# Optimization experiments

Hardware: AMD Instinct MI355X
Metric: run time of the kernel (lower is better)

Reference implementation:

```python
import jax, jax.numpy as jnp
import numpy as np
from jax import lax

POOL_OUT = 20  # SOCA AdaptiveAvgPool2d((20,20))
MID = 16       # out_channel // 2
BN_EPS = 1e-3


def _pool_matrix(n, out):
    # Row-stochastic matrix replicating torch AdaptiveAvgPool2d bin boundaries:
    # start = floor(i*n/out), end = ceil((i+1)*n/out)
    P = np.zeros((out, n), np.float32)
    for i in range(out):
        s = (i * n) // out
        e = -((-(i + 1) * n) // out)
        P[i, s:e] = 1.0 / (e - s)
    return jnp.asarray(P)


def setup_inputs() -> dict:
    key = jax.random.key(0)
    ks = jax.random.split(key, 5)
    B, C, H, W = 16, 256, 128, 128
    OC = 32
    x = jax.random.normal(ks[0], (B, C, H, W), dtype=jnp.float32)
    linear_w = jax.random.normal(ks[1], (C, C), dtype=jnp.float32) * (1.0 / np.sqrt(C))
    linear_b = jnp.zeros((C,), jnp.float32)
    lsa_w = jax.random.normal(ks[2], (1, 2, 7, 7), dtype=jnp.float32) * 0.1  # Conv2d(2,1,7) no bias
    conv_w = jax.random.normal(ks[3], (OC, OC, 3, 3), dtype=jnp.float32) * (1.0 / np.sqrt(OC * 9))
    conv_b = jnp.zeros((OC,), jnp.float32)
    bn_gamma = jnp.ones((OC,), jnp.float32)
    bn_beta = jnp.zeros((OC,), jnp.float32)
    return {"x": x, "linear_w": linear_w, "linear_b": linear_b, "lsa_w": lsa_w,
            "conv_w": conv_w, "conv_b": conv_b, "bn_gamma": bn_gamma, "bn_beta": bn_beta}


def _bsa_forward(x, linear_w, linear_b, lsa_w, conv_w, conv_b, bn_gamma, bn_beta):
    b, c, h, w = x.shape
    # ---- SOCA: second-order channel attention ----
    PH = _pool_matrix(h, POOL_OUT)
    PW = _pool_matrix(w, POOL_OUT)
    xp = jnp.einsum('oh,bchw,pw->bcop', PH, x, PW)          # (b,c,20,20)
    n = POOL_OUT * POOL_OUT
    v = xp.reshape(b, c, n).transpose(0, 2, 1)               # (b,400,c)
    vc = v - v.mean(axis=1, keepdims=True)
    cov = jnp.einsum('bnc,bnd->bcd', vc, vc) / (n - 1)       # (b,c,c)
    feat = cov.mean(axis=2)                                  # (b,c)
    attn = jax.nn.sigmoid(feat @ linear_w.T + linear_b)      # (b,c)
    # ---- channel scoring / top-k selection ----
    score = attn.mean(axis=0)                                # (c,)
    score_id = jnp.argsort(-score)                           # descending
    max_id = jnp.sort(score_id[:MID])                        # (MID,)
    x1 = jnp.take(x, max_id, axis=1) * (1.0 + score[max_id])[None, :, None, None]
    # ---- grouped channel mean (c divisible by MID by construction) ----
    g = c // MID
    x2 = x.reshape(b, MID, g, h, w).mean(axis=2)             # (b,MID,h,w)
    xc = jnp.concatenate([x1, x2], axis=1)                   # (b,32,h,w)
    # ---- LSA spatial attention ----
    s = jnp.concatenate([xc.mean(axis=1, keepdims=True),
                         xc.max(axis=1, keepdims=True)], axis=1)  # (b,2,h,w)
    a = lax.conv_general_dilated(s, lsa_w, (1, 1), [(3, 3), (3, 3)],
                                 dimension_numbers=('NCHW', 'OIHW', 'NCHW'))
    xa = xc * jax.nn.sigmoid(a)
    # ---- CBA: conv(3x3, stride 2) + BN(train stats) + SiLU ----
    y = lax.conv_general_dilated(xa, conv_w, (2, 2), [(1, 1), (1, 1)],
                                 dimension_numbers=('NCHW', 'OIHW', 'NCHW'))
    y = y + conv_b[None, :, None, None]
    mu = y.mean(axis=(0, 2, 3))
    var = y.var(axis=(0, 2, 3))
    yn = (y - mu[None, :, None, None]) * lax.rsqrt(var + BN_EPS)[None, :, None, None]
    yn = yn * bn_gamma[None, :, None, None] + bn_beta[None, :, None, None]
    return yn * jax.nn.sigmoid(yn)  # SiLU


def reference(x, linear_w, linear_b, lsa_w, conv_w, conv_b, bn_gamma, bn_beta):
    return _bsa_forward(x, linear_w, linear_b, lsa_w, conv_w, conv_b, bn_gamma, bn_beta)
```

## Files before the change

### kernel.cpp

```cpp
#include <hip/hip_runtime.h>
#include <math.h>

#define B_ 16
#define C_ 256
#define H_ 128
#define W_ 128
#define HW_ (H_*W_)
#define PO 20
#define NPOOL (PO*PO)
#define MID_ 16
#define OC_ 32
#define OH_ 64
#define OW_ 64
#define BN_EPS 1e-3f

#define OFF_XP     0
#define OFF_SN     1638400
#define OFF_FEAT   1644800
#define OFF_SCORE  1648896
#define OFF_MAXID  1649152
#define OFF_SCALE  1649168
#define OFF_BNSUM  1649184
#define OFF_BNSQ   1649216
#define OFF_SMEAN  1649248
#define OFF_SMAX   1911392
#define OFF_SIGA   2173536
#define OFF_XC     2435680

__device__ __forceinline__ int bin_s(int p) { return (p * 128) / 20; }
__device__ __forceinline__ int bin_e(int p) { return ((p + 1) * 128 + 19) / 20; }

__global__ __launch_bounds__(256) void k_pool2(const float* __restrict__ x,
                                               float* __restrict__ xp,
                                               float* __restrict__ sn,
                                               float* __restrict__ xc) {
  __shared__ float tmp[2][64 * 21];
  const int blk = blockIdx.x;
  const int b = blk >> 5, g = (blk >> 1) & 15, rh = blk & 1;
  const int tid = threadIdx.x;
  const int hl = tid >> 2, q = tid & 3;
  const int hg = rh * 64 + hl;
  const float* rowbase = x + (size_t)(b * C_) * HW_ + (size_t)hg * W_ + q * 32;

  float4 xacc[8];
#pragma unroll
  for (int j = 0; j < 8; ++j) xacc[j] = make_float4(0.f, 0.f, 0.f, 0.f);
  float snacc = 0.f;

  for (int k = 0; k < 16; ++k) {
    const int c = g * 16 + k;
    const float4* src4 = (const float4*)(rowbase + (size_t)c * HW_);
    float bin[5];
#pragma unroll
    for (int p = 0; p < 5; ++p) bin[p] = 0.f;
#pragma unroll
    for (int j = 0; j < 8; ++j) {
      float4 v = src4[j];
      xacc[j].x += v.x; xacc[j].y += v.y; xacc[j].z += v.z; xacc[j].w += v.w;
      const float c4[4] = {v.x, v.y, v.z, v.w};
#pragma unroll
      for (int kk = 0; kk < 4; ++kk) {
        const int cc = 4 * j + kk;
#pragma unroll
        for (int p = 0; p < 5; ++p) {
          const int S = (p * 32) / 5;
          const int E = ((p + 1) * 32 + 4) / 5;
          if (cc >= S && cc < E) bin[p] += c4[kk];
        }
      }
    }
    float* tb = tmp[k & 1];
#pragma unroll
    for (int p = 0; p < 5; ++p) {
      const int S = (p * 32) / 5, E = ((p + 1) * 32 + 4) / 5;
      tb[hl * 21 + q * 5 + p] = bin[p] / (float)(E - S);
    }
    __syncthreads();
    if (tid < 200) {
      const int ol = tid / 20, p = tid % 20;
      const int o = rh * 10 + ol;
      const int rs = bin_s(o), re = bin_e(o);
      float s = 0.f;
      for (int r = rs; r < re; ++r) s += tb[(r - rh * 64) * 21 + p];
      float v = s / (float)(re - rs);
      xp[(size_t)(b * C_ + c) * NPOOL + o * PO + p] = v;
      snacc += v;
    }
  }
  if (tid < 200) atomicAdd(&sn[b * NPOOL + rh * 200 + tid], snacc);
  float4* dst = (float4*)(xc + (size_t)(b * OC_ + MID_ + g) * HW_ + (size_t)hg * W_ + q * 32);
#pragma unroll
  for (int j = 0; j < 8; ++j) {
    float4 v = xacc[j];
    v.x *= 0.0625f; v.y *= 0.0625f; v.z *= 0.0625f; v.w *= 0.0625f;
    dst[j] = v;
  }
}

__global__ __launch_bounds__(256) void k_feat(const float* __restrict__ xp,
                                              const float* __restrict__ sn,
                                              float* __restrict__ feat) {
  const int b = blockIdx.x;
  const int tid = threadIdx.x;
  __shared__ float snl[NPOOL];
  __shared__ float red[256];
  const float4* row4 = (const float4*)(xp + (size_t)(b * C_ + tid) * NPOOL);
  for (int i = tid; i < NPOOL; i += 256) snl[i] = sn[b * NPOOL + i];
  float rs = 0.f;
#pragma unroll 4
  for (int n = 0; n < NPOOL / 4; ++n) {
    float4 v = row4[n];
    rs += v.x + v.y + v.z + v.w;
  }
  red[tid] = rs;
  __syncthreads();
  for (int s = 128; s > 0; s >>= 1) {
    if (tid < s) red[tid] += red[tid + s];
    __syncthreads();
  }
  const float totm = red[0] / (float)NPOOL;
  __syncthreads();
  float sl = 0.f;
  for (int i = tid; i < NPOOL; i += 256) sl += snl[i];
  red[tid] = sl;
  __syncthreads();
  for (int s = 128; s > 0; s >>= 1) {
    if (tid < s) red[tid] += red[tid + s];
    __syncthreads();
  }
  const float S = red[0] - (float)NPOOL * totm;
  float dot = 0.f;
#pragma unroll 4
  for (int n4 = 0; n4 < NPOOL / 4; ++n4) {
    float4 v = row4[n4];
    dot += v.x * snl[4 * n4] + v.y * snl[4 * n4 + 1]
         + v.z * snl[4 * n4 + 2] + v.w * snl[4 * n4 + 3];
  }
  const float m = rs / (float)NPOOL;
  feat[b * C_ + tid] = (dot - totm * rs - m * S) / ((float)(NPOOL - 1) * (float)C_);
}

__global__ __launch_bounds__(256) void k_attn(const float* __restrict__ feat,
                                              const float* __restrict__ lw,
                                              const float* __restrict__ lb,
                                              float* __restrict__ score) {
  __shared__ float sf[B_ * 257];
  __shared__ float wc[16 * 257];
  __shared__ float zs[16 * 17];
  const int tid = threadIdx.x;
  const int j0 = blockIdx.x * 16;
  for (int i = tid; i < B_ * C_; i += 256) sf[(i >> 8) * 257 + (i & 255)] = feat[i];
  for (int i = tid; i < 16 * C_; i += 256)
    wc[(i >> 8) * 257 + (i & 255)] = lw[(size_t)(j0 + (i >> 8)) * C_ + (i & 255)];
  __syncthreads();
  const int jl = tid >> 4, bb = tid & 15;
  float z = 0.f;
#pragma unroll 8
  for (int i = 0; i < C_; ++i) z += sf[bb * 257 + i] * wc[jl * 257 + i];
  z += lb[j0 + jl];
  zs[jl * 17 + bb] = 1.0f / (1.0f + expf(-z));
  __syncthreads();
  if (tid < 16) {
    float s = 0.f;
#pragma unroll
    for (int k = 0; k < 16; ++k) s += zs[tid * 17 + k];
    score[j0 + tid] = s / (float)B_;
  }
}

__global__ __launch_bounds__(256) void k_select(const float* __restrict__ score,
                                                int* __restrict__ max_id,
                                                float* __restrict__ scale,
                                                float* __restrict__ bnzero) {
  __shared__ float ss[C_];
  __shared__ int flag[C_];
  const int tid = threadIdx.x;
  if (tid < 64) bnzero[tid] = 0.f;
  ss[tid] = score[tid];
  __syncthreads();
  float my = ss[tid];
  int rank = 0;
  for (int k = 0; k < C_; ++k) {
    float v = ss[k];
    rank += (v > my || (v == my && k < tid)) ? 1 : 0;
  }
  flag[tid] = (rank < MID_) ? 1 : 0;
  __syncthreads();
  if (rank < MID_) {
    int pos = 0;
    for (int k = 0; k < tid; ++k) pos += flag[k];
    max_id[pos] = tid;
    scale[pos] = 1.0f + my;
  }
}

__global__ __launch_bounds__(256) void k_build(const float* __restrict__ x,
                                               const int* __restrict__ max_id,
                                               const float* __restrict__ scale,
                                               float* __restrict__ xc,
                                               float* __restrict__ smean,
                                               float* __restrict__ smax) {
  __shared__ int mid_s[MID_];
  __shared__ float sc_s[MID_];
  __shared__ float4 ps[128], pm[128];
  const int tid = threadIdx.x;
  if (tid < MID_) {
    mid_s[tid] = max_id[tid];
    sc_s[tid] = scale[tid];
  }
  __syncthreads();
  const int p = tid & 127, s = tid >> 7;
  const int P = blockIdx.x * 128 + p;
  const int b = P >> 12, pix4 = P & 4095;
  const float4* xb = (const float4*)x + (size_t)(b * C_) * (HW_ / 4) + pix4;
  float4* xcb = (float4*)xc + (size_t)(b * OC_) * (HW_ / 4) + pix4;
  float4 ms = make_float4(0.f, 0.f, 0.f, 0.f);
  float4 mx = make_float4(-INFINITY, -INFINITY, -INFINITY, -INFINITY);
#pragma unroll
  for (int mi = 0; mi < 8; ++mi) {
    int m = s * 8 + mi;
    float4 t = xb[(size_t)mid_s[m] * (HW_ / 4)];
    float sc = sc_s[m];
    t.x *= sc; t.y *= sc; t.z *= sc; t.w *= sc;
    xcb[(size_t)m * (HW_ / 4)] = t;
    ms.x += t.x; ms.y += t.y; ms.z += t.z; ms.w += t.w;
    mx.x = fmaxf(mx.x, t.x); mx.y = fmaxf(mx.y, t.y);
    mx.z = fmaxf(mx.z, t.z); mx.w = fmaxf(mx.w, t.w);
  }
#pragma unroll
  for (int gi = 0; gi < 8; ++gi) {
    float4 t = xcb[(size_t)(MID_ + s * 8 + gi) * (HW_ / 4)];
    ms.x += t.x; ms.y += t.y; ms.z += t.z; ms.w += t.w;
    mx.x = fmaxf(mx.x, t.x); mx.y = fmaxf(mx.y, t.y);
    mx.z = fmaxf(mx.z, t.z); mx.w = fmaxf(mx.w, t.w);
  }
  if (s == 1) { ps[p] = ms; pm[p] = mx; }
  __syncthreads();
  if (s == 0) {
    float4 a = ps[p], m2 = pm[p];
    ms.x = (ms.x + a.x) * (1.f / 32.f); ms.y = (ms.y + a.y) * (1.f / 32.f);
    ms.z = (ms.z + a.z) * (1.f / 32.f); ms.w = (ms.w + a.w) * (1.f / 32.f);
    mx.x = fmaxf(mx.x, m2.x); mx.y = fmaxf(mx.y, m2.y);
    mx.z = fmaxf(mx.z, m2.z); mx.w = fmaxf(mx.w, m2.w);
    ((float4*)smean)[P] = ms;
    ((float4*)smax)[P] = mx;
  }
}

__global__ __launch_bounds__(256) void k_lsa(const float* __restrict__ smean,
                                             const float* __restrict__ smax,
                                             const float* __restrict__ lsa_w,
                                             float* __restrict__ siga) {
  __shared__ float w0[49], w1[49];
  if (threadIdx.x < 49) {
    w0[threadIdx.x] = lsa_w[threadIdx.x];
    w1[threadIdx.x] = lsa_w[49 + threadIdx.x];
  }
  __syncthreads();
  int idx = blockIdx.x * 256 + threadIdx.x;
  int b = idx >> 14;
  int pix = idx & (HW_ - 1);
  int h = pix >> 7, w = pix & 127;
  const float* pm = smean + (size_t)b * HW_;
  const float* px = smax + (size_t)b * HW_;
  float acc = 0.f;
  for (int kh = 0; kh < 7; ++kh) {
    int ih = h + kh - 3;
    if (ih < 0 || ih >= H_) continue;
    for (int kw = 0; kw < 7; ++kw) {
      int iw = w + kw - 3;
      if (iw < 0 || iw >= W_) continue;
      int p = ih * W_ + iw;
      acc += pm[p] * w0[kh * 7 + kw] + px[p] * w1[kh * 7 + kw];
    }
  }
  siga[idx] = 1.0f / (1.0f + __expf(-acc));
}

__global__ __launch_bounds__(256) void k_conv(const float* __restrict__ xc,
                                              const float* __restrict__ siga,
                                              const float* __restrict__ conv_w,
                                              const float* __restrict__ conv_b,
                                              float* __restrict__ out,
                                              float* __restrict__ bnsum,
                                              float* __restrict__ bnsq) {
  __shared__ __attribute__((aligned(16))) float in_lds[4 * 5 * 132];
  __shared__ float sg_lds[5 * 132];
  __shared__ float w_lds[288 * 32];
  const int tid = threadIdx.x;
  const int oc = tid & 31;
  const int g = tid >> 5;
  const int b = blockIdx.x >> 5;
  const int oh0 = (blockIdx.x & 31) * 2;
  const int ih0 = 2 * oh0 - 1;

  for (int i = tid; i < 288 * 32; i += 256) {
    int oc_ = i / 288, rem = i % 288;
    w_lds[rem * 32 + oc_] = conv_w[i];
  }
  const float* sgb = siga + (size_t)b * HW_;
  for (int i = tid; i < 5 * 132; i += 256) {
    int r = i / 132, col = i % 132;
    int ih = ih0 + r, iw = col - 1;
    float v = 0.f;
    if (ih >= 0 && ih < H_ && iw >= 0 && iw < W_) v = sgb[ih * W_ + iw];
    sg_lds[i] = v;
  }

  float acc[2][8];
#pragma unroll
  for (int a = 0; a < 2; ++a)
#pragma unroll
    for (int o = 0; o < 8; ++o) acc[a][o] = 0.f;

  for (int chunk = 0; chunk < 8; ++chunk) {
    __syncthreads();
    for (int i = tid; i < 4 * 5 * 132; i += 256) {
      int icl = i / 660;
      int rem = i % 660;
      int r = rem / 132, col = rem % 132;
      int ih = ih0 + r, iw = col - 1;
      float v = 0.f;
      if (ih >= 0 && ih < H_ && iw >= 0 && iw < W_) {
        v = xc[((size_t)(b * OC_) + (chunk * 4 + icl)) * HW_ + ih * W_ + iw] * sg_lds[rem];
      }
      in_lds[i] = v;
    }
    __syncthreads();
#pragma unroll
    for (int icl = 0; icl < 4; ++icl) {
      const int wb = (chunk * 4 + icl) * 9 * 32 + oc;
#pragma unroll
      for (int r = 0; r < 5; ++r) {
        float f[20] __attribute__((aligned(16)));
        const float4* s4 = (const float4*)&in_lds[(icl * 5 + r) * 132 + 16 * g];
#pragma unroll
        for (int j = 0; j < 5; ++j) ((float4*)f)[j] = s4[j];
#pragma unroll
        for (int ohl = 0; ohl < 2; ++ohl) {
          const int kh = r - 2 * ohl;
          if (kh < 0 || kh > 2) continue;
          float w0 = w_lds[wb + (kh * 3 + 0) * 32];
          float w1 = w_lds[wb + (kh * 3 + 1) * 32];
          float w2 = w_lds[wb + (kh * 3 + 2) * 32];
#pragma unroll
          for (int o = 0; o < 8; ++o)
            acc[ohl][o] += f[2 * o] * w0 + f[2 * o + 1] * w1 + f[2 * o + 2] * w2;
        }
      }
    }
  }

  float bias = conv_b[oc];
  float lsum = 0.f, lsq = 0.f;
  float* outp = out + ((size_t)(b * OC_) + oc) * (OH_ * OW_) + (size_t)oh0 * OW_ + g * 8;
#pragma unroll
  for (int ohl = 0; ohl < 2; ++ohl) {
    float vout[8] __attribute__((aligned(16)));
#pragma unroll
    for (int o = 0; o < 8; ++o) {
      float v = acc[ohl][o] + bias;
      vout[o] = v;
      lsum += v;
      lsq += v * v;
    }
    *((float4*)(outp + ohl * OW_)) = *(float4*)&vout[0];
    *((float4*)(outp + ohl * OW_ + 4)) = *(float4*)&vout[4];
  }
  __syncthreads();
  in_lds[tid] = lsum;
  in_lds[256 + tid] = lsq;
  __syncthreads();
  if (tid < 32) {
    float t = 0.f, tq = 0.f;
#pragma unroll
    for (int gg = 0; gg < 8; ++gg) {
      t += in_lds[gg * 32 + tid];
      tq += in_lds[256 + gg * 32 + tid];
    }
    atomicAdd(&bnsum[tid], t);
    atomicAdd(&bnsq[tid], tq);
  }
}

__global__ __launch_bounds__(256) void k_apply(float* __restrict__ out,
                                               const float* __restrict__ sum,
                                               const float* __restrict__ sq,
                                               const float* __restrict__ gamma,
                                               const float* __restrict__ beta) {
  __shared__ float ssc[OC_], ssh[OC_];
  if (threadIdx.x < OC_) {
    int i = threadIdx.x;
    const float N = (float)(B_ * OH_ * OW_);
    float mu = sum[i] / N;
    float var = sq[i] / N - mu * mu;
    float sc = gamma[i] / sqrtf(var + BN_EPS);
    ssc[i] = sc;
    ssh[i] = beta[i] - mu * sc;
  }
  __syncthreads();
  int idx4 = blockIdx.x * 256 + threadIdx.x;
  int oc = (idx4 >> 10) & 31;
  float sc = ssc[oc], sh = ssh[oc];
  float4 v = ((float4*)out)[idx4];
  float t;
  t = v.x * sc + sh; v.x = t / (1.0f + __expf(-t));
  t = v.y * sc + sh; v.y = t / (1.0f + __expf(-t));
  t = v.z * sc + sh; v.z = t / (1.0f + __expf(-t));
  t = v.w * sc + sh; v.w = t / (1.0f + __expf(-t));
  ((float4*)out)[idx4] = v;
}

extern "C" void kernel_launch(void* const* d_in, const int* in_sizes, int n_in,
                              void* d_out, int out_size, void* d_ws, size_t ws_size,
                              hipStream_t stream) {
  const float* x      = (const float*)d_in[0];
  const float* lw     = (const float*)d_in[1];
  const float* lb     = (const float*)d_in[2];
  const float* lsa_w  = (const float*)d_in[3];
  const float* conv_w = (const float*)d_in[4];
  const float* conv_b = (const float*)d_in[5];
  const float* gamma  = (const float*)d_in[6];
  const float* beta   = (const float*)d_in[7];
  float* out = (float*)d_out;
  float* ws = (float*)d_ws;

  hipMemsetAsync(ws + OFF_SN, 0, B_ * NPOOL * sizeof(float), stream);

  k_pool2<<<512, 256, 0, stream>>>(x, ws + OFF_XP, ws + OFF_SN, ws + OFF_XC);
  k_feat<<<B_, 256, 0, stream>>>(ws + OFF_XP, ws + OFF_SN, ws + OFF_FEAT);
  k_attn<<<16, 256, 0, stream>>>(ws + OFF_FEAT, lw, lb, ws + OFF_SCORE);
  k_select<<<1, 256, 0, stream>>>(ws + OFF_SCORE, (int*)(ws + OFF_MAXID),
                                  ws + OFF_SCALE, ws + OFF_BNSUM);
  k_build<<<512, 256, 0, stream>>>(x, (const int*)(ws + OFF_MAXID), ws + OFF_SCALE,
                                   ws + OFF_XC, ws + OFF_SMEAN, ws + OFF_SMAX);
  k_lsa<<<1024, 256, 0, stream>>>(ws + OFF_SMEAN, ws + OFF_SMAX, lsa_w, ws + OFF_SIGA);
  k_conv<<<512, 256, 0, stream>>>(ws + OFF_XC, ws + OFF_SIGA, conv_w, conv_b, out,
                                  ws + OFF_BNSUM, ws + OFF_BNSQ);
  k_apply<<<2048, 256, 0, stream>>>(out, ws + OFF_BNSUM, ws + OFF_BNSQ, gamma, beta);
}
```

Before: 517.7 us.

## Fuse feat/attn/select kernels, prefetch pooling loads, pad conv weight LDS

Merges the covariance-feature and linear/sigmoid attention kernels into one per-batch kernel that accumulates the score with atomics. It also moves top-k selection into every k_build block, which removes two tiny launches but repeats the rank computation in 512 blocks. The pooling kernel now software-prefetches the next channel's rows into registers and uses a lighter barrier. The conv kernel pads its weight LDS to stride 33 and caches the 9 taps in registers. A single memset now zeroes the sn, score and BN accumulators, and the feature formula drops the S term, which is zero in exact arithmetic.

```diff
diff --git a/kernel.cpp b/kernel.cpp
--- a/kernel.cpp
+++ b/kernel.cpp
@@ -16,10 +16,7 @@
 
 #define OFF_XP     0
 #define OFF_SN     1638400
-#define OFF_FEAT   1644800
 #define OFF_SCORE  1648896
-#define OFF_MAXID  1649152
-#define OFF_SCALE  1649168
 #define OFF_BNSUM  1649184
 #define OFF_BNSQ   1649216
 #define OFF_SMEAN  1649248
@@ -47,15 +44,27 @@
   for (int j = 0; j < 8; ++j) xacc[j] = make_float4(0.f, 0.f, 0.f, 0.f);
   float snacc = 0.f;
 
+  float4 cur[8], nxt[8];
+  {
+    const float4* s4 = (const float4*)(rowbase + (size_t)(g * 16) * HW_);
+#pragma unroll
+    for (int j = 0; j < 8; ++j) cur[j] = s4[j];
+  }
+
+#pragma unroll
   for (int k = 0; k < 16; ++k) {
+    if (k < 15) {
+      const float4* s4 = (const float4*)(rowbase + (size_t)(g * 16 + k + 1) * HW_);
+#pragma unroll
+      for (int j = 0; j < 8; ++j) nxt[j] = s4[j];
+    }
     const int c = g * 16 + k;
-    const float4* src4 = (const float4*)(rowbase + (size_t)c * HW_);
     float bin[5];
 #pragma unroll
     for (int p = 0; p < 5; ++p) bin[p] = 0.f;
 #pragma unroll
     for (int j = 0; j < 8; ++j) {
-      float4 v = src4[j];
+      float4 v = cur[j];
       xacc[j].x += v.x; xacc[j].y += v.y; xacc[j].z += v.z; xacc[j].w += v.w;
       const float c4[4] = {v.x, v.y, v.z, v.w};
 #pragma unroll
@@ -75,16 +84,20 @@
       const int S = (p * 32) / 5, E = ((p + 1) * 32 + 4) / 5;
       tb[hl * 21 + q * 5 + p] = bin[p] / (float)(E - S);
     }
-    __syncthreads();
+    asm volatile("s_waitcnt lgkmcnt(0)\n\ts_barrier" ::: "memory");
     if (tid < 200) {
       const int ol = tid / 20, p = tid % 20;
       const int o = rh * 10 + ol;
-      const int rs = bin_s(o), re = bin_e(o);
+      const int rs_ = bin_s(o), re_ = bin_e(o);
       float s = 0.f;
-      for (int r = rs; r < re; ++r) s += tb[(r - rh * 64) * 21 + p];
-      float v = s / (float)(re - rs);
+      for (int r = rs_; r < re_; ++r) s += tb[(r - rh * 64) * 21 + p];
+      float v = s / (float)(re_ - rs_);
       xp[(size_t)(b * C_ + c) * NPOOL + o * PO + p] = v;
       snacc += v;
+    }
+    if (k < 15) {
+#pragma unroll
+      for (int j = 0; j < 8; ++j) cur[j] = nxt[j];
     }
   }
   if (tid < 200) atomicAdd(&sn[b * NPOOL + rh * 200 + tid], snacc);
@@ -97,20 +110,26 @@
   }
 }
 
-__global__ __launch_bounds__(256) void k_feat(const float* __restrict__ xp,
-                                              const float* __restrict__ sn,
-                                              float* __restrict__ feat) {
+__global__ __launch_bounds__(256) void k_featattn(const float* __restrict__ xp,
+                                                  const float* __restrict__ sn,
+                                                  const float* __restrict__ lw,
+                                                  const float* __restrict__ lb,
+                                                  float* __restrict__ score) {
   const int b = blockIdx.x;
   const int tid = threadIdx.x;
   __shared__ float snl[NPOOL];
   __shared__ float red[256];
+  __shared__ float featl[C_];
+  for (int i = tid; i < NPOOL; i += 256) snl[i] = sn[b * NPOOL + i];
+  __syncthreads();
   const float4* row4 = (const float4*)(xp + (size_t)(b * C_ + tid) * NPOOL);
-  for (int i = tid; i < NPOOL; i += 256) snl[i] = sn[b * NPOOL + i];
-  float rs = 0.f;
+  float rs = 0.f, dot = 0.f;
 #pragma unroll 4
   for (int n = 0; n < NPOOL / 4; ++n) {
     float4 v = row4[n];
     rs += v.x + v.y + v.z + v.w;
+    dot += v.x * snl[4 * n] + v.y * snl[4 * n + 1]
+         + v.z * snl[4 * n + 2] + v.w * snl[4 * n + 3];
   }
   red[tid] = rs;
   __syncthreads();
@@ -119,94 +138,49 @@
     __syncthreads();
   }
   const float totm = red[0] / (float)NPOOL;
-  __syncthreads();
-  float sl = 0.f;
-  for (int i = tid; i < NPOOL; i += 256) sl += snl[i];
-  red[tid] = sl;
-  __syncthreads();
-  for (int s = 128; s > 0; s >>= 1) {
-    if (tid < s) red[tid] += red[tid + s];
-    __syncthreads();
-  }
-  const float S = red[0] - (float)NPOOL * totm;
-  float dot = 0.f;
+  featl[tid] = (dot - totm * rs) / ((float)(NPOOL - 1) * (float)C_);
+  __syncthreads();
+  const float4* wrow = (const float4*)(lw + (size_t)tid * C_);
+  float z = 0.f;
 #pragma unroll 4
-  for (int n4 = 0; n4 < NPOOL / 4; ++n4) {
-    float4 v = row4[n4];
-    dot += v.x * snl[4 * n4] + v.y * snl[4 * n4 + 1]
-         + v.z * snl[4 * n4 + 2] + v.w * snl[4 * n4 + 3];
-  }
-  const float m = rs / (float)NPOOL;
-  feat[b * C_ + tid] = (dot - totm * rs - m * S) / ((float)(NPOOL - 1) * (float)C_);
-}
-
-__global__ __launch_bounds__(256) void k_attn(const float* __restrict__ feat,
-                                              const float* __restrict__ lw,
-                                              const float* __restrict__ lb,
-                                              float* __restrict__ score) {
-  __shared__ float sf[B_ * 257];
-  __shared__ float wc[16 * 257];
-  __shared__ float zs[16 * 17];
-  const int tid = threadIdx.x;
-  const int j0 = blockIdx.x * 16;
-  for (int i = tid; i < B_ * C_; i += 256) sf[(i >> 8) * 257 + (i & 255)] = feat[i];
-  for (int i = tid; i < 16 * C_; i += 256)
-    wc[(i >> 8) * 257 + (i & 255)] = lw[(size_t)(j0 + (i >> 8)) * C_ + (i & 255)];
-  __syncthreads();
-  const int jl = tid >> 4, bb = tid & 15;
-  float z = 0.f;
-#pragma unroll 8
-  for (int i = 0; i < C_; ++i) z += sf[bb * 257 + i] * wc[jl * 257 + i];
-  z += lb[j0 + jl];
-  zs[jl * 17 + bb] = 1.0f / (1.0f + expf(-z));
-  __syncthreads();
-  if (tid < 16) {
-    float s = 0.f;
-#pragma unroll
-    for (int k = 0; k < 16; ++k) s += zs[tid * 17 + k];
-    score[j0 + tid] = s / (float)B_;
-  }
-}
-
-__global__ __launch_bounds__(256) void k_select(const float* __restrict__ score,
-                                                int* __restrict__ max_id,
-                                                float* __restrict__ scale,
-                                                float* __restrict__ bnzero) {
-  __shared__ float ss[C_];
-  __shared__ int flag[C_];
-  const int tid = threadIdx.x;
-  if (tid < 64) bnzero[tid] = 0.f;
-  ss[tid] = score[tid];
-  __syncthreads();
-  float my = ss[tid];
-  int rank = 0;
-  for (int k = 0; k < C_; ++k) {
-    float v = ss[k];
-    rank += (v > my || (v == my && k < tid)) ? 1 : 0;
-  }
-  flag[tid] = (rank < MID_) ? 1 : 0;
-  __syncthreads();
-  if (rank < MID_) {
-    int pos = 0;
-    for (int k = 0; k < tid; ++k) pos += flag[k];
-    max_id[pos] = tid;
-    scale[pos] = 1.0f + my;
-  }
+  for (int i = 0; i < C_ / 4; ++i) {
+    float4 w = wrow[i];
+    z += w.x * featl[4 * i] + w.y * featl[4 * i + 1]
+       + w.z * featl[4 * i + 2] + w.w * featl[4 * i + 3];
+  }
+  z += lb[tid];
+  float sig = 1.0f / (1.0f + expf(-z));
+  atomicAdd(&score[tid], sig * (1.0f / (float)B_));
 }
 
 __global__ __launch_bounds__(256) void k_build(const float* __restrict__ x,
-                                               const int* __restrict__ max_id,
-                                               const float* __restrict__ scale,
+                                               const float* __restrict__ score,
                                                float* __restrict__ xc,
                                                float* __restrict__ smean,
                                                float* __restrict__ smax) {
+  __shared__ float ss[C_];
+  __shared__ int flag[C_];
   __shared__ int mid_s[MID_];
   __shared__ float sc_s[MID_];
   __shared__ float4 ps[128], pm[128];
   const int tid = threadIdx.x;
-  if (tid < MID_) {
-    mid_s[tid] = max_id[tid];
-    sc_s[tid] = scale[tid];
+  ss[tid] = score[tid];
+  __syncthreads();
+  {
+    float my = ss[tid];
+    int rank = 0;
+    for (int k = 0; k < C_; ++k) {
+      float v = ss[k];
+      rank += (v > my || (v == my && k < tid)) ? 1 : 0;
+    }
+    flag[tid] = (rank < MID_) ? 1 : 0;
+    __syncthreads();
+    if (rank < MID_) {
+      int pos = 0;
+      for (int k = 0; k < tid; ++k) pos += flag[k];
+      mid_s[pos] = tid;
+      sc_s[pos] = 1.0f + my;
+    }
   }
   __syncthreads();
   const int p = tid & 127, s = tid >> 7;
@@ -286,7 +260,7 @@
                                               float* __restrict__ bnsq) {
   __shared__ __attribute__((aligned(16))) float in_lds[4 * 5 * 132];
   __shared__ float sg_lds[5 * 132];
-  __shared__ float w_lds[288 * 32];
+  __shared__ float w_lds[288 * 33];
   const int tid = threadIdx.x;
   const int oc = tid & 31;
   const int g = tid >> 5;
@@ -296,7 +270,7 @@
 
   for (int i = tid; i < 288 * 32; i += 256) {
     int oc_ = i / 288, rem = i % 288;
-    w_lds[rem * 32 + oc_] = conv_w[i];
+    w_lds[rem * 33 + oc_] = conv_w[i];
   }
   const float* sgb = siga + (size_t)b * HW_;
   for (int i = tid; i < 5 * 132; i += 256) {
@@ -329,7 +303,10 @@
     __syncthreads();
 #pragma unroll
     for (int icl = 0; icl < 4; ++icl) {
-      const int wb = (chunk * 4 + icl) * 9 * 32 + oc;
+      float wr[9];
+      const int wb = (chunk * 4 + icl) * 9 * 33 + oc;
+#pragma unroll
+      for (int t = 0; t < 9; ++t) wr[t] = w_lds[wb + t * 33];
 #pragma unroll
       for (int r = 0; r < 5; ++r) {
         float f[20] __attribute__((aligned(16)));
@@ -340,9 +317,9 @@
         for (int ohl = 0; ohl < 2; ++ohl) {
           const int kh = r - 2 * ohl;
           if (kh < 0 || kh > 2) continue;
-          float w0 = w_lds[wb + (kh * 3 + 0) * 32];
-          float w1 = w_lds[wb + (kh * 3 + 1) * 32];
-          float w2 = w_lds[wb + (kh * 3 + 2) * 32];
+          float w0 = wr[kh * 3 + 0];
+          float w1 = wr[kh * 3 + 1];
+          float w2 = wr[kh * 3 + 2];
 #pragma unroll
           for (int o = 0; o < 8; ++o)
             acc[ohl][o] += f[2 * o] * w0 + f[2 * o + 1] * w1 + f[2 * o + 2] * w2;
@@ -425,15 +402,13 @@
   float* out = (float*)d_out;
   float* ws = (float*)d_ws;
 
-  hipMemsetAsync(ws + OFF_SN, 0, B_ * NPOOL * sizeof(float), stream);
+  hipMemsetAsync(ws + OFF_SN, 0,
+                 (size_t)(OFF_BNSQ + OC_ - OFF_SN) * sizeof(float), stream);
 
   k_pool2<<<512, 256, 0, stream>>>(x, ws + OFF_XP, ws + OFF_SN, ws + OFF_XC);
-  k_feat<<<B_, 256, 0, stream>>>(ws + OFF_XP, ws + OFF_SN, ws + OFF_FEAT);
-  k_attn<<<16, 256, 0, stream>>>(ws + OFF_FEAT, lw, lb, ws + OFF_SCORE);
-  k_select<<<1, 256, 0, stream>>>(ws + OFF_SCORE, (int*)(ws + OFF_MAXID),
-                                  ws + OFF_SCALE, ws + OFF_BNSUM);
-  k_build<<<512, 256, 0, stream>>>(x, (const int*)(ws + OFF_MAXID), ws + OFF_SCALE,
-                                   ws + OFF_XC, ws + OFF_SMEAN, ws + OFF_SMAX);
+  k_featattn<<<B_, 256, 0, stream>>>(ws + OFF_XP, ws + OFF_SN, lw, lb, ws + OFF_SCORE);
+  k_build<<<512, 256, 0, stream>>>(x, ws + OFF_SCORE, ws + OFF_XC,
+                                   ws + OFF_SMEAN, ws + OFF_SMAX);
   k_lsa<<<1024, 256, 0, stream>>>(ws + OFF_SMEAN, ws + OFF_SMAX, lsa_w, ws + OFF_SIGA);
   k_conv<<<512, 256, 0, stream>>>(ws + OFF_XC, ws + OFF_SIGA, conv_w, conv_b, out,
                                   ws + OFF_BNSUM, ws + OFF_BNSQ);
```

Measured after the change: 504.2 us. 2.6% less time.
